# Performance work log

Hardware: AMD Instinct MI355X
Metric: run time of the kernel (lower is better)

The kernel has to match this reference:

```python
import jax, jax.numpy as jnp
import numpy as np

B, S, K, N = 4, 2048, 4096, 11008
GROUP_SIZE = 128
NUM_GROUPS = K // GROUP_SIZE  # 32


def setup_inputs() -> dict:
    key = jax.random.key(0)
    k1, k2, k3, k4, k5 = jax.random.split(key, 5)
    x = jax.random.normal(k1, (B, S, K), dtype=jnp.float32)
    # sensitivity-sorted column order is a permutation of [0, K)
    col_indices = jax.random.permutation(k2, K).astype(jnp.int32)
    # packed uint8 nibbles stored as int32 in [0, 256)
    w_packed = jax.random.randint(k3, (K // 2, N), 0, 256, dtype=jnp.int32)
    # per-group, per-output-column dequant scales (positive, small)
    scales = (jax.random.uniform(k4, (NUM_GROUPS, N), dtype=jnp.float32) + 0.05) * 0.01
    bias = jax.random.normal(k5, (N,), dtype=jnp.float32) * 0.01
    return {"x": x, "col_indices": col_indices, "w_packed": w_packed,
            "scales": scales, "bias": bias}


def _dequant_weight(w_packed, scales):
    # unpack int4 nibbles: low nibble -> even k, high nibble -> odd k
    low = (w_packed & 15) - 8          # [K//2, N]
    high = ((w_packed >> 4) & 15) - 8  # [K//2, N]
    w_int = jnp.stack([low, high], axis=1).reshape(K, N)  # interleaved [K, N]
    # per-group dequant: scale index = k // group_size
    w = w_int.astype(scales.dtype).reshape(NUM_GROUPS, GROUP_SIZE, N)
    w = w * scales[:, None, :]
    return w.reshape(K, N)


def reference(x, col_indices, w_packed, scales, bias):
    orig_shape = x.shape
    xm = x.reshape(-1, K)                     # [M, K]
    xg = jnp.take(xm, col_indices, axis=1)    # column-reorder gather [M, K]
    w = _dequant_weight(w_packed, scales)     # [K, N]
    out = jnp.einsum('mk,kn->mn', xg, w)      # fp32 accumulate
    out = out + bias
    return out.reshape(orig_shape[0], orig_shape[1], N)
```

## Files before the change

### kernel.cpp

```cpp
#include <hip/hip_runtime.h>
#include <hip/hip_bf16.h>
#include <stdint.h>

#define M_DIM 8192
#define K_DIM 4096
#define N_DIM 11008
#define NKT   (K_DIM / 64)
#define NIT   (NKT / 2)

typedef __attribute__((ext_vector_type(8))) short bf16x8;
typedef __attribute__((ext_vector_type(4))) float f32x4;
typedef __attribute__((ext_vector_type(4))) unsigned int uint4v;

__device__ __forceinline__ unsigned short f2bf(float f) {
    __hip_bfloat16 h = __float2bfloat16(f);
    return __builtin_bit_cast(unsigned short, h);
}

__device__ __forceinline__ void gload_lds16(const unsigned short* g, unsigned short* l) {
    __builtin_amdgcn_global_load_lds(
        (const __attribute__((address_space(1))) void*)g,
        (__attribute__((address_space(3))) void*)l,
        16, 0, 0);
}

__device__ __forceinline__ unsigned lds_addr(const unsigned short* p) {
    return (unsigned)(uintptr_t)(const __attribute__((address_space(3))) unsigned short*)p;
}

#define DSR(dst, a, OFF) asm volatile("ds_read_b128 %0, %1 offset:" OFF \
    : "=v"(dst) : "v"(a) : "memory")

__device__ __forceinline__ void ld_quad(bf16x8* d, unsigned a) {
    DSR(d[0], a, "0");
    DSR(d[1], a, "1024");
    DSR(d[2], a, "2048");
    DSR(d[3], a, "3072");
}

__global__ void permute_x_kernel(const float* __restrict__ x,
                                 const int* __restrict__ ci,
                                 unsigned short* __restrict__ xg) {
    int idx = blockIdx.x * 256 + threadIdx.x;
    int64_t base = (int64_t)idx * 4;
    int m = (int)(base >> 12);
    int k = (int)(base & 4095);
    const float* xrow = x + ((int64_t)m << 12);
    int4 c4 = *reinterpret_cast<const int4*>(ci + k);
    ushort4 o;
    o.x = f2bf(xrow[c4.x]);
    o.y = f2bf(xrow[c4.y]);
    o.z = f2bf(xrow[c4.z]);
    o.w = f2bf(xrow[c4.w]);
    *reinterpret_cast<ushort4*>(xg + base) = o;
}

__global__ void dequant_w_kernel(const int* __restrict__ wp,
                                 const float* __restrict__ scales,
                                 unsigned short* __restrict__ wT) {
    __shared__ unsigned short tile[64][65];
    int n0 = blockIdx.x * 64;
    int k0 = blockIdx.y * 64;
    int g = k0 >> 7;
    int t = threadIdx.x;
    int col = t & 63;
    int r0 = t >> 6;
    float s = scales[(int64_t)g * N_DIM + n0 + col];
    int pr0 = k0 >> 1;
#pragma unroll
    for (int i = 0; i < 8; ++i) {
        int row = r0 + i * 4;
        int p = wp[(int64_t)(pr0 + row) * N_DIM + n0 + col];
        tile[2 * row][col]     = f2bf((float)((p & 15) - 8) * s);
        tile[2 * row + 1][col] = f2bf((float)(((p >> 4) & 15) - 8) * s);
    }
    __syncthreads();
    int nl = t >> 2;
    int kk0 = (t & 3) << 4;
    unsigned short vals[16];
#pragma unroll
    for (int j = 0; j < 16; ++j) vals[j] = tile[kk0 + j][nl];
    uint4v* dst = reinterpret_cast<uint4v*>(wT + (int64_t)(n0 + nl) * K_DIM + k0 + kk0);
    dst[0] = *reinterpret_cast<const uint4v*>(&vals[0]);
    dst[1] = *reinterpret_cast<const uint4v*>(&vals[8]);
}


template <int MB>
__device__ __forceinline__ void mfma_blk(f32x4 (&acc)[8][4], const bf16x8 (&av)[8],
                                         const bf16x8 (&bv)[4]) {
    __builtin_amdgcn_s_setprio(1);
#pragma unroll
    for (int m = 0; m < 4; ++m)
#pragma unroll
        for (int n = 0; n < 4; ++n)
            acc[MB + m][n] = __builtin_amdgcn_mfma_f32_16x16x32_bf16(
                av[MB + m], bv[n], acc[MB + m][n], 0, 0, 0);
    __builtin_amdgcn_s_setprio(0);
}

template <int BUF, int ISB, int KK>
__device__ __forceinline__ void stage(const unsigned short* __restrict__ G, int row0,
                                      int kt, unsigned short* lds,
                                      int w32, int riw, int s8, int wLds) {
    if (kt < NKT) {
#pragma unroll
        for (int j = 0; j < 2; ++j) {
            const unsigned short* src =
                G + (int64_t)(row0 + w32 + j * 16 + riw) * K_DIM + kt * 64 + KK * 32 + s8;
            gload_lds16(src, lds + BUF * 32768 + ISB * 16384 + KK * 8192 + wLds + j * 512);
        }
    }
}

#define BAR() do { __builtin_amdgcn_s_barrier(); asm volatile("" ::: "memory"); } while (0)
#define LGKM(N) do { \
    asm volatile("s_waitcnt lgkmcnt(" #N ")" ::: "memory"); \
    __builtin_amdgcn_sched_barrier(0); \
} while (0)

__global__ __launch_bounds__(512, 2)
void gemm_kernel(const unsigned short* __restrict__ A,
                 const unsigned short* __restrict__ BT,
                 const float* __restrict__ bias,
                 float* __restrict__ C) {
    __shared__ unsigned short lds[65536];

    constexpr int NT = N_DIM / 256;
    int wg = blockIdx.x, nwg = gridDim.x;
    int q = nwg >> 3, r = nwg & 7;
    int xcd = wg & 7, li = wg >> 3;
    int swz = (xcd < r ? xcd * (q + 1) : r * (q + 1) + (xcd - r) * q) + li;
    int by = swz / NT, bx = swz - by * NT;
    int brow = by << 8, bcol = bx << 8;

    int t = threadIdx.x;
    int lane = t & 63, w = t >> 6;
    int wr = w >> 2, wc = w & 3;
    int fr = lane & 15, fq = lane >> 4;

    const unsigned xr = (unsigned)((fr & 6) << 3);

    const int riw = lane >> 2;
    const int s8 = ((lane & 3) ^ ((lane >> 3) & 3)) << 3;
    const int w32 = w * 32, wLds = w * 1024;

    const unsigned aA0 = (lds_addr(lds) + (unsigned)((wr * 128 + fr) * 64 + fq * 16)) ^ xr;
    const unsigned bA0 = (lds_addr(lds) + 32768u + (unsigned)((wc * 64 + fr) * 64 + fq * 16)) ^ xr;
    const unsigned aA1 = aA0 + 65536;
    const unsigned bA1 = bA0 + 65536;

    f32x4 acc[8][4];
#pragma unroll
    for (int m = 0; m < 8; ++m)
#pragma unroll
        for (int n = 0; n < 4; ++n) acc[m][n] = (f32x4){0.f, 0.f, 0.f, 0.f};

    stage<0, 0, 0>(A,  brow, 0, lds, w32, riw, s8, wLds);
    stage<0, 0, 1>(A,  brow, 0, lds, w32, riw, s8, wLds);
    stage<0, 1, 0>(BT, bcol, 0, lds, w32, riw, s8, wLds);
    stage<0, 1, 1>(BT, bcol, 0, lds, w32, riw, s8, wLds);
    stage<1, 1, 0>(BT, bcol, 1, lds, w32, riw, s8, wLds);
    stage<1, 0, 0>(A,  brow, 1, lds, w32, riw, s8, wLds);
    stage<1, 1, 1>(BT, bcol, 1, lds, w32, riw, s8, wLds);
    asm volatile("s_waitcnt vmcnt(6)" ::: "memory");
    BAR();

#pragma unroll 1
    for (int it = 0; it < NIT; ++it) {
        const int t1 = 2 * it + 1, t2 = 2 * it + 2, t3 = 2 * it + 3;
        const bool lastIt = (it == NIT - 1);
        bf16x8 a0[8], a1[8], b0[4], b1[4];

        ld_quad(&a0[0], aA0);
        ld_quad(&b0[0], bA0);
        ld_quad(&a0[4], aA0 + 4096);
        ld_quad(&a1[0], aA0 + 16384);
        stage<1, 0, 1>(A, brow, t1, lds, w32, riw, s8, wLds);
        LGKM(8);
        mfma_blk<0>(acc, a0, b0);
        BAR();

        ld_quad(&a1[4], aA0 + 20480);
        ld_quad(&b1[0], bA0 + 16384);
        stage<0, 1, 0>(BT, bcol, t2, lds, w32, riw, s8, wLds);
        LGKM(8);
        mfma_blk<4>(acc, a0, b0);
        BAR();

        stage<0, 0, 0>(A, brow, t2, lds, w32, riw, s8, wLds);
        LGKM(0);
        mfma_blk<0>(acc, a1, b1);
        BAR();

        stage<0, 1, 1>(BT, bcol, t2, lds, w32, riw, s8, wLds);
        mfma_blk<4>(acc, a1, b1);
        if (!lastIt) asm volatile("s_waitcnt vmcnt(6)" ::: "memory");
        else         asm volatile("s_waitcnt vmcnt(0)" ::: "memory");
        BAR();

        ld_quad(&a0[0], aA1);
        ld_quad(&b0[0], bA1);
        ld_quad(&a0[4], aA1 + 4096);
        ld_quad(&a1[0], aA1 + 16384);
        stage<0, 0, 1>(A, brow, t2, lds, w32, riw, s8, wLds);
        LGKM(8);
        mfma_blk<0>(acc, a0, b0);
        BAR();

        ld_quad(&a1[4], aA1 + 20480);
        ld_quad(&b1[0], bA1 + 16384);
        stage<1, 1, 0>(BT, bcol, t3, lds, w32, riw, s8, wLds);
        LGKM(8);
        mfma_blk<4>(acc, a0, b0);
        BAR();

        stage<1, 0, 0>(A, brow, t3, lds, w32, riw, s8, wLds);
        LGKM(0);
        mfma_blk<0>(acc, a1, b1);
        BAR();

        stage<1, 1, 1>(BT, bcol, t3, lds, w32, riw, s8, wLds);
        mfma_blk<4>(acc, a1, b1);
        if (!lastIt) asm volatile("s_waitcnt vmcnt(6)" ::: "memory");
        BAR();
    }

    int orow0 = brow + wr * 128 + fq * 4;
    int ocol0 = bcol + wc * 64 + fr;
#pragma unroll
    for (int n = 0; n < 4; ++n) {
        int col = ocol0 + n * 16;
        float bval = bias[col];
#pragma unroll
        for (int m = 0; m < 8; ++m) {
            int row = orow0 + m * 16;
            float* cp = C + (int64_t)row * N_DIM + col;
#pragma unroll
            for (int j = 0; j < 4; ++j) {
                cp[(int64_t)j * N_DIM] = acc[m][n][j] + bval;
            }
        }
    }
}

extern "C" void kernel_launch(void* const* d_in, const int* in_sizes, int n_in,
                              void* d_out, int out_size, void* d_ws, size_t ws_size,
                              hipStream_t stream) {
    const float* x      = (const float*)d_in[0];
    const int* ci       = (const int*)d_in[1];
    const int* wp       = (const int*)d_in[2];
    const float* scales = (const float*)d_in[3];
    const float* bias   = (const float*)d_in[4];
    float* out          = (float*)d_out;

    const size_t wT_bytes = (size_t)N_DIM * K_DIM * 2;
    unsigned short* wT = (unsigned short*)d_ws;
    unsigned short* xg = wT + (size_t)N_DIM * K_DIM;

    size_t cap = (ws_size > wT_bytes) ? (ws_size - wT_bytes) : 0;
    int max_rows = (int)(cap / ((size_t)K_DIM * 2));
    int chunk_rows = (max_rows / 256) * 256;
    if (chunk_rows <= 0) chunk_rows = 256;
    if (chunk_rows > M_DIM) chunk_rows = M_DIM;

    dequant_w_kernel<<<dim3(N_DIM / 64, K_DIM / 64), 256, 0, stream>>>(wp, scales, wT);

    for (int m0 = 0; m0 < M_DIM; m0 += chunk_rows) {
        int rows = M_DIM - m0 < chunk_rows ? M_DIM - m0 : chunk_rows;
        int pgrid = (int)(((int64_t)rows * K_DIM) / (4 * 256));
        permute_x_kernel<<<pgrid, 256, 0, stream>>>(
            x + (int64_t)m0 * K_DIM, ci, xg);
        int grid = (rows / 256) * (N_DIM / 256);
        gemm_kernel<<<grid, 512, 0, stream>>>(
            xg, wT, bias, out + (int64_t)m0 * N_DIM);
    }
}
```

Before: 847.6 us.

## Restructure GEMM main loop into triple-buffered 32-wide K tiles

Replaces the double-buffered 64-wide K-tile schedule with a triple-buffered ring of 32-wide K tiles. Each tile is processed in two phases that interleave LDS fragment reads, async global-to-LDS loads and MFMA blocks. Buffer offsets are precomputed as immediates, and global source pointers are hoisted out of the loop. This cuts LDS use and live fragment registers and aims for finer-grained overlap of loads with MFMA work. The cost is twice as many barriers per unit of K, which could expose more synchronization stalls.

```diff
diff --git a/kernel.cpp b/kernel.cpp
--- a/kernel.cpp
+++ b/kernel.cpp
@@ -5,8 +5,7 @@
 #define M_DIM 8192
 #define K_DIM 4096
 #define N_DIM 11008
-#define NKT   (K_DIM / 64)
-#define NIT   (NKT / 2)
+#define NT32  128
 
 typedef __attribute__((ext_vector_type(8))) short bf16x8;
 typedef __attribute__((ext_vector_type(4))) float f32x4;
@@ -28,15 +27,14 @@
     return (unsigned)(uintptr_t)(const __attribute__((address_space(3))) unsigned short*)p;
 }
 
-#define DSR(dst, a, OFF) asm volatile("ds_read_b128 %0, %1 offset:" OFF \
-    : "=v"(dst) : "v"(a) : "memory")
-
-__device__ __forceinline__ void ld_quad(bf16x8* d, unsigned a) {
-    DSR(d[0], a, "0");
-    DSR(d[1], a, "1024");
-    DSR(d[2], a, "2048");
-    DSR(d[3], a, "3072");
-}
+#define DSRI(dst, a, OFF) asm volatile("ds_read_b128 %0, %1 offset:%2" \
+    : "=v"(dst) : "v"(a), "n"(OFF) : "memory")
+
+#define LGKM(N) do { \
+    asm volatile("s_waitcnt lgkmcnt(" #N ")" ::: "memory"); \
+    __builtin_amdgcn_sched_barrier(0); \
+} while (0)
+#define BAR() do { __builtin_amdgcn_s_barrier(); asm volatile("" ::: "memory"); } while (0)
 
 __global__ void permute_x_kernel(const float* __restrict__ x,
                                  const int* __restrict__ ci,
@@ -86,45 +84,77 @@
 }
 
 
+template <int BUF>
+__device__ __forceinline__ void read_RA(bf16x8 (&a)[4], bf16x8 (&b)[4],
+                                        unsigned aA01, unsigned aA2,
+                                        unsigned bB01, unsigned bB2) {
+    const unsigned ad = (BUF < 2) ? aA01 : aA2;
+    const unsigned bd = (BUF < 2) ? bB01 : bB2;
+    constexpr int bo = (BUF < 2) ? BUF * 32768 : 0;
+    DSRI(a[0], ad, bo + 0);
+    DSRI(a[1], ad, bo + 1024);
+    DSRI(a[2], ad, bo + 2048);
+    DSRI(a[3], ad, bo + 3072);
+    DSRI(b[0], bd, bo + 0);
+    DSRI(b[1], bd, bo + 1024);
+    DSRI(b[2], bd, bo + 2048);
+    DSRI(b[3], bd, bo + 3072);
+}
+
+template <int BUF>
+__device__ __forceinline__ void read_RB(bf16x8 (&a2)[4], unsigned aA01, unsigned aA2) {
+    const unsigned ad = (BUF < 2) ? aA01 : aA2;
+    constexpr int bo = (BUF < 2) ? BUF * 32768 : 0;
+    DSRI(a2[0], ad, bo + 4096);
+    DSRI(a2[1], ad, bo + 5120);
+    DSRI(a2[2], ad, bo + 6144);
+    DSRI(a2[3], ad, bo + 7168);
+}
+
 template <int MB>
-__device__ __forceinline__ void mfma_blk(f32x4 (&acc)[8][4], const bf16x8 (&av)[8],
-                                         const bf16x8 (&bv)[4]) {
+__device__ __forceinline__ void mfma4(f32x4 (&acc)[8][4], const bf16x8 (&av)[4],
+                                      const bf16x8 (&bv)[4]) {
     __builtin_amdgcn_s_setprio(1);
 #pragma unroll
     for (int m = 0; m < 4; ++m)
 #pragma unroll
         for (int n = 0; n < 4; ++n)
             acc[MB + m][n] = __builtin_amdgcn_mfma_f32_16x16x32_bf16(
-                av[MB + m], bv[n], acc[MB + m][n], 0, 0, 0);
+                av[m], bv[n], acc[MB + m][n], 0, 0, 0);
     __builtin_amdgcn_s_setprio(0);
 }
 
-template <int BUF, int ISB, int KK>
-__device__ __forceinline__ void stage(const unsigned short* __restrict__ G, int row0,
-                                      int kt, unsigned short* lds,
-                                      int w32, int riw, int s8, int wLds) {
-    if (kt < NKT) {
-#pragma unroll
-        for (int j = 0; j < 2; ++j) {
-            const unsigned short* src =
-                G + (int64_t)(row0 + w32 + j * 16 + riw) * K_DIM + kt * 64 + KK * 32 + s8;
-            gload_lds16(src, lds + BUF * 32768 + ISB * 16384 + KK * 8192 + wLds + j * 512);
-        }
-    }
-}
-
-#define BAR() do { __builtin_amdgcn_s_barrier(); asm volatile("" ::: "memory"); } while (0)
-#define LGKM(N) do { \
-    asm volatile("s_waitcnt lgkmcnt(" #N ")" ::: "memory"); \
-    __builtin_amdgcn_sched_barrier(0); \
-} while (0)
+template <int DBUF, int ISB>
+__device__ __forceinline__ void stage2(const unsigned short* p0, const unsigned short* p1,
+                                       int t, unsigned short* lds, int wLds) {
+    const unsigned short* s0 = p0 + t * 32;
+    const unsigned short* s1 = p1 + t * 32;
+    unsigned short* d = lds + DBUF * 16384 + ISB * 8192 + wLds;
+    gload_lds16(s0, d);
+    gload_lds16(s1, d + 512);
+}
+
+#define PH_TILE(B, BN, BS, CA_, CB_, NA_, NB_, tt)                        \
+    do {                                                                  \
+        read_RB<B>(a2, aA01, aA2);                                        \
+        stage2<BS, 0>(pA0, pA1, (tt), lds, wLds);                         \
+        LGKM(4);                                                          \
+        mfma4<0>(acc, CA_, CB_);                                          \
+        asm volatile("s_waitcnt vmcnt(2)" ::: "memory");                  \
+        BAR();                                                            \
+        read_RA<BN>(NA_, NB_, aA01, aA2, bB01, bB2);                      \
+        stage2<BS, 1>(pB0, pB1, (tt), lds, wLds);                         \
+        LGKM(8);                                                          \
+        mfma4<4>(acc, a2, CB_);                                           \
+        BAR();                                                            \
+    } while (0)
 
 __global__ __launch_bounds__(512, 2)
 void gemm_kernel(const unsigned short* __restrict__ A,
                  const unsigned short* __restrict__ BT,
                  const float* __restrict__ bias,
                  float* __restrict__ C) {
-    __shared__ unsigned short lds[65536];
+    __shared__ unsigned short lds[49152];
 
     constexpr int NT = N_DIM / 256;
     int wg = blockIdx.x, nwg = gridDim.x;
@@ -140,15 +170,20 @@
     int fr = lane & 15, fq = lane >> 4;
 
     const unsigned xr = (unsigned)((fr & 6) << 3);
-
     const int riw = lane >> 2;
     const int s8 = ((lane & 3) ^ ((lane >> 3) & 3)) << 3;
     const int w32 = w * 32, wLds = w * 1024;
 
-    const unsigned aA0 = (lds_addr(lds) + (unsigned)((wr * 128 + fr) * 64 + fq * 16)) ^ xr;
-    const unsigned bA0 = (lds_addr(lds) + 32768u + (unsigned)((wc * 64 + fr) * 64 + fq * 16)) ^ xr;
-    const unsigned aA1 = aA0 + 65536;
-    const unsigned bA1 = bA0 + 65536;
+    const unsigned ldsB = lds_addr(lds);
+    const unsigned aA01 = ldsB + ((unsigned)((wr * 128 + fr) * 64 + fq * 16) ^ xr);
+    const unsigned bB01 = ldsB + 16384u + ((unsigned)((wc * 64 + fr) * 64 + fq * 16) ^ xr);
+    const unsigned aA2 = aA01 + 65536;
+    const unsigned bB2 = bB01 + 65536;
+
+    const unsigned short* pA0 = A + (int64_t)(brow + w32 + riw) * K_DIM + s8;
+    const unsigned short* pA1 = pA0 + 16 * K_DIM;
+    const unsigned short* pB0 = BT + (int64_t)(bcol + w32 + riw) * K_DIM + s8;
+    const unsigned short* pB1 = pB0 + 16 * K_DIM;
 
     f32x4 acc[8][4];
 #pragma unroll
@@ -156,75 +191,41 @@
 #pragma unroll
         for (int n = 0; n < 4; ++n) acc[m][n] = (f32x4){0.f, 0.f, 0.f, 0.f};
 
-    stage<0, 0, 0>(A,  brow, 0, lds, w32, riw, s8, wLds);
-    stage<0, 0, 1>(A,  brow, 0, lds, w32, riw, s8, wLds);
-    stage<0, 1, 0>(BT, bcol, 0, lds, w32, riw, s8, wLds);
-    stage<0, 1, 1>(BT, bcol, 0, lds, w32, riw, s8, wLds);
-    stage<1, 1, 0>(BT, bcol, 1, lds, w32, riw, s8, wLds);
-    stage<1, 0, 0>(A,  brow, 1, lds, w32, riw, s8, wLds);
-    stage<1, 1, 1>(BT, bcol, 1, lds, w32, riw, s8, wLds);
-    asm volatile("s_waitcnt vmcnt(6)" ::: "memory");
+    bf16x8 aX[4], bX[4], aY[4], bY[4], a2[4];
+
+    stage2<0, 0>(pA0, pA1, 0, lds, wLds);
+    stage2<0, 1>(pB0, pB1, 0, lds, wLds);
+    stage2<1, 0>(pA0, pA1, 1, lds, wLds);
+    stage2<1, 1>(pB0, pB1, 1, lds, wLds);
+    asm volatile("s_waitcnt vmcnt(4)" ::: "memory");
     BAR();
+    read_RA<0>(aX, bX, aA01, aA2, bB01, bB2);
 
 #pragma unroll 1
-    for (int it = 0; it < NIT; ++it) {
-        const int t1 = 2 * it + 1, t2 = 2 * it + 2, t3 = 2 * it + 3;
-        const bool lastIt = (it == NIT - 1);
-        bf16x8 a0[8], a1[8], b0[4], b1[4];
-
-        ld_quad(&a0[0], aA0);
-        ld_quad(&b0[0], bA0);
-        ld_quad(&a0[4], aA0 + 4096);
-        ld_quad(&a1[0], aA0 + 16384);
-        stage<1, 0, 1>(A, brow, t1, lds, w32, riw, s8, wLds);
-        LGKM(8);
-        mfma_blk<0>(acc, a0, b0);
-        BAR();
-
-        ld_quad(&a1[4], aA0 + 20480);
-        ld_quad(&b1[0], bA0 + 16384);
-        stage<0, 1, 0>(BT, bcol, t2, lds, w32, riw, s8, wLds);
-        LGKM(8);
-        mfma_blk<4>(acc, a0, b0);
-        BAR();
-
-        stage<0, 0, 0>(A, brow, t2, lds, w32, riw, s8, wLds);
-        LGKM(0);
-        mfma_blk<0>(acc, a1, b1);
-        BAR();
-
-        stage<0, 1, 1>(BT, bcol, t2, lds, w32, riw, s8, wLds);
-        mfma_blk<4>(acc, a1, b1);
-        if (!lastIt) asm volatile("s_waitcnt vmcnt(6)" ::: "memory");
-        else         asm volatile("s_waitcnt vmcnt(0)" ::: "memory");
-        BAR();
-
-        ld_quad(&a0[0], aA1);
-        ld_quad(&b0[0], bA1);
-        ld_quad(&a0[4], aA1 + 4096);
-        ld_quad(&a1[0], aA1 + 16384);
-        stage<0, 0, 1>(A, brow, t2, lds, w32, riw, s8, wLds);
-        LGKM(8);
-        mfma_blk<0>(acc, a0, b0);
-        BAR();
-
-        ld_quad(&a1[4], aA1 + 20480);
-        ld_quad(&b1[0], bA1 + 16384);
-        stage<1, 1, 0>(BT, bcol, t3, lds, w32, riw, s8, wLds);
-        LGKM(8);
-        mfma_blk<4>(acc, a0, b0);
-        BAR();
-
-        stage<1, 0, 0>(A, brow, t3, lds, w32, riw, s8, wLds);
-        LGKM(0);
-        mfma_blk<0>(acc, a1, b1);
-        BAR();
-
-        stage<1, 1, 1>(BT, bcol, t3, lds, w32, riw, s8, wLds);
-        mfma_blk<4>(acc, a1, b1);
-        if (!lastIt) asm volatile("s_waitcnt vmcnt(6)" ::: "memory");
-        BAR();
-    }
+    for (int body = 0; body < 21; ++body) {
+        const int t2 = body * 6 + 2;
+        PH_TILE(0, 1, 2, aX, bX, aY, bY, t2);
+        PH_TILE(1, 2, 0, aY, bY, aX, bX, t2 + 1);
+        PH_TILE(2, 0, 1, aX, bX, aY, bY, t2 + 2);
+        PH_TILE(0, 1, 2, aY, bY, aX, bX, t2 + 3);
+        PH_TILE(1, 2, 0, aX, bX, aY, bY, t2 + 4);
+        PH_TILE(2, 0, 1, aY, bY, aX, bX, t2 + 5);
+    }
+
+    read_RB<0>(a2, aA01, aA2);
+    LGKM(4);
+    mfma4<0>(acc, aX, bX);
+    asm volatile("s_waitcnt vmcnt(0)" ::: "memory");
+    BAR();
+    read_RA<1>(aY, bY, aA01, aA2, bB01, bB2);
+    LGKM(8);
+    mfma4<4>(acc, a2, bX);
+    BAR();
+    read_RB<1>(a2, aA01, aA2);
+    LGKM(4);
+    mfma4<0>(acc, aY, bY);
+    LGKM(0);
+    mfma4<4>(acc, a2, bY);
 
     int orow0 = brow + wr * 128 + fq * 4;
     int ocol0 = bcol + wc * 64 + fr;
```

Measured after the change: 833.7 us. No clear change (-1.6%).
